# Performance work log

Hardware: AMD Instinct MI355X
Metric: run time of the kernel (lower is better)

## Reference

```python
import jax, jax.numpy as jnp
import numpy as np

H = 256

def setup_inputs() -> dict:
    key = jax.random.key(0)
    ks = jax.random.split(key, 8)
    B, S = 32, 4096
    hidden = jax.random.normal(ks[0], (B, H), dtype=jnp.float32)
    encoder_outputs = jax.random.normal(ks[1], (B, S, H), dtype=jnp.float32)
    scale = 1.0 / np.sqrt(H)
    W1_w = jax.random.uniform(ks[2], (H, H), jnp.float32, -scale, scale)
    W1_b = jax.random.uniform(ks[3], (H,), jnp.float32, -scale, scale)
    W2_w = jax.random.uniform(ks[4], (H, H), jnp.float32, -scale, scale)
    W2_b = jax.random.uniform(ks[5], (H,), jnp.float32, -scale, scale)
    V_w = jax.random.uniform(ks[6], (H, 1), jnp.float32, -scale, scale)
    V_b = jax.random.uniform(ks[7], (1,), jnp.float32, -scale, scale)
    return {"hidden": hidden, "encoder_outputs": encoder_outputs,
            "W1_w": W1_w, "W1_b": W1_b, "W2_w": W2_w, "W2_b": W2_b,
            "V_w": V_w, "V_b": V_b}

def reference(hidden, encoder_outputs, W1_w, W1_b, W2_w, W2_b, V_w, V_b):
    # hidden: (B,H), encoder_outputs: (B,S,H)
    q = hidden @ W1_w + W1_b                     # (B,H)
    k = jnp.einsum('bsh,hd->bsd', encoder_outputs, W2_w) + W2_b  # (B,S,H)
    energy = jnp.tanh(q[:, None, :] + k)         # (B,S,H)
    scores = jnp.einsum('bsh,ho->bso', energy, V_w) + V_b        # (B,S,1)
    attention_weights = jax.nn.softmax(scores, axis=1)           # (B,S,1)
    context_vector = jnp.einsum('bso,bsh->bh', attention_weights, encoder_outputs)  # (B,H)
    return attention_weights, context_vector
```

## Files before the change

### kernel.cpp

```cpp
#include <hip/hip_runtime.h>
#include <hip/hip_bf16.h>
#include <math.h>

#define BB 32
#define SS 4096
#define HH 256

typedef __bf16 bf16x8 __attribute__((ext_vector_type(8)));
typedef float f32x4 __attribute__((ext_vector_type(4)));

#define GLOBAL_AS __attribute__((address_space(1)))
#define LDS_AS    __attribute__((address_space(3)))

__device__ inline bf16x8 cvt8(const float4& x, const float4& y) {
    union { __hip_bfloat162 p[4]; bf16x8 v; } u;
    u.p[0] = __float22bfloat162_rn(make_float2(x.x, x.y));
    u.p[1] = __float22bfloat162_rn(make_float2(x.z, x.w));
    u.p[2] = __float22bfloat162_rn(make_float2(y.x, y.y));
    u.p[3] = __float22bfloat162_rn(make_float2(y.z, y.w));
    return u.v;
}

__device__ inline float fast_tanh(float x) {
    float xc = fminf(fmaxf(x, -10.f), 10.f);
    float e  = __expf(2.f * xc);
    return (e - 1.f) * __builtin_amdgcn_rcpf(e + 1.f);
}

__global__ void prep_kernel(const float* __restrict__ W2_w,
                            ushort* __restrict__ w2sw,
                            const float* __restrict__ hidden,
                            const float* __restrict__ W1_w,
                            const float* __restrict__ W1_b,
                            const float* __restrict__ W2_b,
                            float* __restrict__ qq) {
    __shared__ float hid[HH];
    const int t = threadIdx.x;
    if (blockIdx.x < 256) {
        const int i = blockIdx.x * 256 + t;
        const int j    = i & 7;
        const int lane = (i >> 3) & 63;
        const int nt   = (i >> 9) & 15;
        const int kc   = i >> 13;
        const int k = kc * 32 + ((lane >> 4) & 3) * 8 + j;
        const int n = nt * 16 + (lane & 15);
        __hip_bfloat16 h = __float2bfloat16(W2_w[k * HH + n]);
        w2sw[i] = *(ushort*)&h;
    } else {
        const int b = blockIdx.x - 256;
        hid[t] = hidden[b * HH + t];
        __syncthreads();
        float acc = 0.f;
#pragma unroll 16
        for (int k = 0; k < HH; ++k)
            acc = fmaf(hid[k], W1_w[k * HH + t], acc);
        qq[b * HH + t] = acc + W1_b[t] + W2_b[t];
    }
}

__global__ __launch_bounds__(256, 4)
void score_kernel(const float* __restrict__ enc,
                  const ushort* __restrict__ w2sw,
                  const float* __restrict__ qq,
                  const float* __restrict__ V_w,
                  const float* __restrict__ V_b,
                  float* __restrict__ scores,
                  float* __restrict__ mlpart) {
    __shared__ ushort w2buf[2][8192];
    __shared__ float sc_lds[64];

    const int t    = threadIdx.x;
    const int b    = blockIdx.y;
    const int s0   = blockIdx.x * 64;
    const int wave = t >> 6;
    const int lane = t & 63;
    const int mw   = wave & 1;
    const int nw   = wave >> 1;
    const int l15  = lane & 15;
    const int quad = lane >> 4;

    f32x4 acc[2][8];
#pragma unroll
    for (int mt = 0; mt < 2; ++mt)
#pragma unroll
        for (int nt = 0; nt < 8; ++nt) acc[mt][nt] = (f32x4)0.f;

    {
        const char* gsrc = (const char*)w2sw + t * 16;
        char* ldst = (char*)&w2buf[0][0] + wave * 1024;
#pragma unroll
        for (int i = 0; i < 4; ++i)
            __builtin_amdgcn_global_load_lds(
                (const GLOBAL_AS void*)(gsrc + i * 4096),
                (LDS_AS void*)(ldst + i * 4096), 16, 0, 0);
    }

    const float* aptr0 =
        enc + ((size_t)(b * SS + s0 + mw * 32 + l15)) * HH + quad * 8;
    const float* aptr1 = aptr0 + (size_t)16 * HH;
    float4 ax0 = *(const float4*)aptr0, ay0 = *(const float4*)(aptr0 + 4);
    float4 ax1 = *(const float4*)aptr1, ay1 = *(const float4*)(aptr1 + 4);

    for (int kc = 0; kc < 8; ++kc) {
        const int cur = kc & 1;
        __syncthreads();
        if (kc < 7) {
            const char* gsrc = (const char*)w2sw + (kc + 1) * 16384 + t * 16;
            char* ldst = (char*)&w2buf[cur ^ 1][0] + wave * 1024;
#pragma unroll
            for (int i = 0; i < 4; ++i)
                __builtin_amdgcn_global_load_lds(
                    (const GLOBAL_AS void*)(gsrc + i * 4096),
                    (LDS_AS void*)(ldst + i * 4096), 16, 0, 0);
        }
        bf16x8 af0 = cvt8(ax0, ay0);
        bf16x8 af1 = cvt8(ax1, ay1);
        if (kc < 7) {
            const int o = (kc + 1) * 32;
            ax0 = *(const float4*)(aptr0 + o);
            ay0 = *(const float4*)(aptr0 + o + 4);
            ax1 = *(const float4*)(aptr1 + o);
            ay1 = *(const float4*)(aptr1 + o + 4);
        }
#pragma unroll
        for (int nt = 0; nt < 8; ++nt) {
            bf16x8 bf =
                *(const bf16x8*)&w2buf[cur][((nw * 8 + nt) * 64 + lane) * 8];
            acc[0][nt] = __builtin_amdgcn_mfma_f32_16x16x32_bf16(af0, bf, acc[0][nt], 0, 0, 0);
            acc[1][nt] = __builtin_amdgcn_mfma_f32_16x16x32_bf16(af1, bf, acc[1][nt], 0, 0, 0);
        }
    }

    float p[2][4] = {{0.f, 0.f, 0.f, 0.f}, {0.f, 0.f, 0.f, 0.f}};
#pragma unroll
    for (int nt = 0; nt < 8; ++nt) {
        const int n = nw * 128 + nt * 16 + l15;
        const float qn = qq[b * HH + n];
        const float vn = V_w[n];
#pragma unroll
        for (int mt = 0; mt < 2; ++mt)
#pragma unroll
            for (int r = 0; r < 4; ++r)
                p[mt][r] = fmaf(vn, fast_tanh(qn + acc[mt][nt][r]), p[mt][r]);
    }
#pragma unroll
    for (int off = 1; off < 16; off <<= 1)
#pragma unroll
        for (int mt = 0; mt < 2; ++mt)
#pragma unroll
            for (int r = 0; r < 4; ++r)
                p[mt][r] += __shfl_xor(p[mt][r], off);

    if (nw == 0 && l15 == 0) {
#pragma unroll
        for (int mt = 0; mt < 2; ++mt)
            *(float4*)&sc_lds[mw * 32 + mt * 16 + quad * 4] =
                make_float4(p[mt][0], p[mt][1], p[mt][2], p[mt][3]);
    }
    __syncthreads();
    const float vb = V_b[0];
    if (nw == 1 && l15 == 0) {
#pragma unroll
        for (int mt = 0; mt < 2; ++mt) {
            const int row = mw * 32 + mt * 16 + quad * 4;
            float4 h = *(const float4*)&sc_lds[row];
            float4 v = make_float4(h.x + p[mt][0] + vb, h.y + p[mt][1] + vb,
                                   h.z + p[mt][2] + vb, h.w + p[mt][3] + vb);
            *(float4*)&sc_lds[row] = v;
            *(float4*)&scores[b * SS + s0 + row] = v;
        }
    }
    __syncthreads();

    if (t < 64) {
        const float v = sc_lds[t];
        float m = v;
#pragma unroll
        for (int off = 1; off < 64; off <<= 1)
            m = fmaxf(m, __shfl_xor(m, off));
        float e = __expf(v - m);
#pragma unroll
        for (int off = 1; off < 64; off <<= 1)
            e += __shfl_xor(e, off);
        if (t == 0) {
            mlpart[(b * 64 + blockIdx.x) * 2]     = m;
            mlpart[(b * 64 + blockIdx.x) * 2 + 1] = e;
        }
    }
}

__global__ __launch_bounds__(256)
void ctx_kernel(const float* __restrict__ scores,
                const float* __restrict__ mlpart,
                const float* __restrict__ enc,
                float* __restrict__ weights_out,
                float* __restrict__ ctx_out) {
    __shared__ float wlds[64];
    __shared__ float accl[4][HH];
    __shared__ float mg_s, linv_s;

    const int t  = threadIdx.x;
    const int b  = blockIdx.y;
    const int c  = blockIdx.x;
    const int s0 = c * 64;

    if (t < 64) {
        const float2 ml = ((const float2*)mlpart)[b * 64 + t];
        float m = ml.x;
#pragma unroll
        for (int off = 1; off < 64; off <<= 1)
            m = fmaxf(m, __shfl_xor(m, off));
        float l = ml.y * __expf(ml.x - m);
#pragma unroll
        for (int off = 1; off < 64; off <<= 1)
            l += __shfl_xor(l, off);
        if (t == 0) { mg_s = m; linv_s = 1.f / l; }
    }
    __syncthreads();
    const float mg = mg_s, linv = linv_s;

    if (t < 64) {
        const float w = __expf(scores[b * SS + s0 + t] - mg) * linv;
        weights_out[b * SS + s0 + t] = w;
        wlds[t] = w;
    }
    __syncthreads();

    const int tr = t >> 6;
    const int h0 = (t & 63) * 4;
    float4 a = make_float4(0.f, 0.f, 0.f, 0.f);
    const float* ep = enc + ((size_t)(b * SS + s0)) * HH;
#pragma unroll
    for (int jj = 0; jj < 16; ++jj) {
        const int j = jj * 4 + tr;
        const float4 e = *(const float4*)(ep + (size_t)j * HH + h0);
        const float w = wlds[j];
        a.x = fmaf(w, e.x, a.x);
        a.y = fmaf(w, e.y, a.y);
        a.z = fmaf(w, e.z, a.z);
        a.w = fmaf(w, e.w, a.w);
    }
    *(float4*)&accl[tr][h0] = a;
    __syncthreads();

    const float s = accl[0][t] + accl[1][t] + accl[2][t] + accl[3][t];
    atomicAdd(&ctx_out[b * HH + t], s);
}

extern "C" void kernel_launch(void* const* d_in, const int* in_sizes, int n_in,
                              void* d_out, int out_size, void* d_ws, size_t ws_size,
                              hipStream_t stream) {
    const float* hidden = (const float*)d_in[0];
    const float* enc    = (const float*)d_in[1];
    const float* W1_w   = (const float*)d_in[2];
    const float* W1_b   = (const float*)d_in[3];
    const float* W2_w   = (const float*)d_in[4];
    const float* W2_b   = (const float*)d_in[5];
    const float* V_w    = (const float*)d_in[6];
    const float* V_b    = (const float*)d_in[7];

    float* out_weights = (float*)d_out;
    float* out_ctx     = (float*)d_out + BB * SS;

    float* ws     = (float*)d_ws;
    float* ws_qq  = ws;
    float* ws_sc  = ws_qq + BB * HH;
    float* ws_ml  = ws_sc + BB * SS;
    ushort* ws_w2 = (ushort*)(ws_ml + BB * 64 * 2);

    hipMemsetAsync(out_ctx, 0, BB * HH * sizeof(float), stream);
    prep_kernel<<<dim3(256 + BB), dim3(256), 0, stream>>>(
        W2_w, ws_w2, hidden, W1_w, W1_b, W2_b, ws_qq);
    score_kernel<<<dim3(SS / 64, BB), dim3(256), 0, stream>>>(
        enc, ws_w2, ws_qq, V_w, V_b, ws_sc, ws_ml);
    ctx_kernel<<<dim3(64, BB), dim3(256), 0, stream>>>(
        ws_sc, ws_ml, enc, out_weights, out_ctx);
}
```

Before: 255.2 us.

## Fuse score and context passes using a static softmax max bound

Uses sum(|V_w|) as an upper bound on every score (tanh is bounded by 1), so each block can exponentiate its scores right away without a global max pass. This lets the score kernel also do the weighted sum over its encoder tile while that tile is likely still in cache, removing the second full read of encoder_outputs. Per-block partial contexts go to a workspace, and a small finish kernel normalises the weights and sums the partials, replacing the memset and the atomics. V_b is dropped because it cancels in the softmax. The risk is underflow in exp if the real scores fall far below the bound.

```diff
diff --git a/kernel.cpp b/kernel.cpp
--- a/kernel.cpp
+++ b/kernel.cpp
@@ -33,8 +33,10 @@
                             const float* __restrict__ W1_w,
                             const float* __restrict__ W1_b,
                             const float* __restrict__ W2_b,
-                            float* __restrict__ qq) {
-    __shared__ float hid[HH];
+                            const float* __restrict__ V_w,
+                            float* __restrict__ qq,
+                            float* __restrict__ Mout) {
+    __shared__ float red[HH];
     const int t = threadIdx.x;
     if (blockIdx.x < 256) {
         const int i = blockIdx.x * 256 + t;
@@ -46,32 +48,42 @@
         const int n = nt * 16 + (lane & 15);
         __hip_bfloat16 h = __float2bfloat16(W2_w[k * HH + n]);
         w2sw[i] = *(ushort*)&h;
-    } else {
+    } else if (blockIdx.x < 256 + BB) {
         const int b = blockIdx.x - 256;
-        hid[t] = hidden[b * HH + t];
+        red[t] = hidden[b * HH + t];
         __syncthreads();
         float acc = 0.f;
 #pragma unroll 16
         for (int k = 0; k < HH; ++k)
-            acc = fmaf(hid[k], W1_w[k * HH + t], acc);
+            acc = fmaf(red[k], W1_w[k * HH + t], acc);
         qq[b * HH + t] = acc + W1_b[t] + W2_b[t];
+    } else {
+        red[t] = fabsf(V_w[t]);
+        __syncthreads();
+        for (int off = 128; off > 0; off >>= 1) {
+            if (t < off) red[t] += red[t + off];
+            __syncthreads();
+        }
+        if (t == 0) Mout[0] = red[0];
     }
 }
 
 __global__ __launch_bounds__(256, 4)
-void score_kernel(const float* __restrict__ enc,
-                  const ushort* __restrict__ w2sw,
-                  const float* __restrict__ qq,
-                  const float* __restrict__ V_w,
-                  const float* __restrict__ V_b,
-                  float* __restrict__ scores,
-                  float* __restrict__ mlpart) {
+void score_ctx_kernel(const float* __restrict__ enc,
+                      const ushort* __restrict__ w2sw,
+                      const float* __restrict__ qq,
+                      const float* __restrict__ V_w,
+                      const float* __restrict__ Mptr,
+                      float* __restrict__ wtilde,
+                      float* __restrict__ part) {
     __shared__ ushort w2buf[2][8192];
     __shared__ float sc_lds[64];
+    __shared__ float accl[4][HH];
 
     const int t    = threadIdx.x;
     const int b    = blockIdx.y;
-    const int s0   = blockIdx.x * 64;
+    const int c    = blockIdx.x;
+    const int s0   = c * 64;
     const int wave = t >> 6;
     const int lane = t & 63;
     const int mw   = wave & 1;
@@ -158,71 +170,19 @@
                 make_float4(p[mt][0], p[mt][1], p[mt][2], p[mt][3]);
     }
     __syncthreads();
-    const float vb = V_b[0];
+    const float Mv = Mptr[0];
     if (nw == 1 && l15 == 0) {
 #pragma unroll
         for (int mt = 0; mt < 2; ++mt) {
             const int row = mw * 32 + mt * 16 + quad * 4;
             float4 h = *(const float4*)&sc_lds[row];
-            float4 v = make_float4(h.x + p[mt][0] + vb, h.y + p[mt][1] + vb,
-                                   h.z + p[mt][2] + vb, h.w + p[mt][3] + vb);
+            float4 v = make_float4(__expf(h.x + p[mt][0] - Mv),
+                                   __expf(h.y + p[mt][1] - Mv),
+                                   __expf(h.z + p[mt][2] - Mv),
+                                   __expf(h.w + p[mt][3] - Mv));
             *(float4*)&sc_lds[row] = v;
-            *(float4*)&scores[b * SS + s0 + row] = v;
-        }
-    }
-    __syncthreads();
-
-    if (t < 64) {
-        const float v = sc_lds[t];
-        float m = v;
-#pragma unroll
-        for (int off = 1; off < 64; off <<= 1)
-            m = fmaxf(m, __shfl_xor(m, off));
-        float e = __expf(v - m);
-#pragma unroll
-        for (int off = 1; off < 64; off <<= 1)
-            e += __shfl_xor(e, off);
-        if (t == 0) {
-            mlpart[(b * 64 + blockIdx.x) * 2]     = m;
-            mlpart[(b * 64 + blockIdx.x) * 2 + 1] = e;
-        }
-    }
-}
-
-__global__ __launch_bounds__(256)
-void ctx_kernel(const float* __restrict__ scores,
-                const float* __restrict__ mlpart,
-                const float* __restrict__ enc,
-                float* __restrict__ weights_out,
-                float* __restrict__ ctx_out) {
-    __shared__ float wlds[64];
-    __shared__ float accl[4][HH];
-    __shared__ float mg_s, linv_s;
-
-    const int t  = threadIdx.x;
-    const int b  = blockIdx.y;
-    const int c  = blockIdx.x;
-    const int s0 = c * 64;
-
-    if (t < 64) {
-        const float2 ml = ((const float2*)mlpart)[b * 64 + t];
-        float m = ml.x;
-#pragma unroll
-        for (int off = 1; off < 64; off <<= 1)
-            m = fmaxf(m, __shfl_xor(m, off));
-        float l = ml.y * __expf(ml.x - m);
-#pragma unroll
-        for (int off = 1; off < 64; off <<= 1)
-            l += __shfl_xor(l, off);
-        if (t == 0) { mg_s = m; linv_s = 1.f / l; }
-    }
-    __syncthreads();
-    const float mg = mg_s, linv = linv_s;
-
-    if (t < 64) {
-        const float w = __expf(scores[b * SS + s0 + t] - mg) * linv;
-        weights_out[b * SS + s0 + t] = w;
-        wlds[t] = w;
+            *(float4*)&wtilde[b * SS + s0 + row] = v;
+        }
     }
     __syncthreads();
 
@@ -234,7 +194,7 @@
     for (int jj = 0; jj < 16; ++jj) {
         const int j = jj * 4 + tr;
         const float4 e = *(const float4*)(ep + (size_t)j * HH + h0);
-        const float w = wlds[j];
+        const float w = sc_lds[j];
         a.x = fmaf(w, e.x, a.x);
         a.y = fmaf(w, e.y, a.y);
         a.z = fmaf(w, e.z, a.z);
@@ -243,8 +203,51 @@
     *(float4*)&accl[tr][h0] = a;
     __syncthreads();
 
-    const float s = accl[0][t] + accl[1][t] + accl[2][t] + accl[3][t];
-    atomicAdd(&ctx_out[b * HH + t], s);
+    part[((size_t)(b * 64 + c)) * HH + t] =
+        accl[0][t] + accl[1][t] + accl[2][t] + accl[3][t];
+}
+
+__global__ __launch_bounds__(256)
+void finish_kernel(const float* __restrict__ wtilde,
+                   const float* __restrict__ part,
+                   float* __restrict__ weights_out,
+                   float* __restrict__ ctx_out) {
+    __shared__ float red[256];
+    __shared__ float linv_s;
+    const int b = blockIdx.x;
+    const int t = threadIdx.x;
+
+    const float4* wt4 = (const float4*)(wtilde + (size_t)b * SS);
+    float4 vals[4];
+    float l = 0.f;
+#pragma unroll
+    for (int i = 0; i < 4; ++i) {
+        vals[i] = wt4[i * 256 + t];
+        l += vals[i].x + vals[i].y + vals[i].z + vals[i].w;
+    }
+    red[t] = l;
+    __syncthreads();
+    for (int off = 128; off > 0; off >>= 1) {
+        if (t < off) red[t] += red[t + off];
+        __syncthreads();
+    }
+    if (t == 0) linv_s = 1.f / red[0];
+    __syncthreads();
+    const float linv = linv_s;
+
+    float4* wo4 = (float4*)(weights_out + (size_t)b * SS);
+#pragma unroll
+    for (int i = 0; i < 4; ++i) {
+        const float4 v = vals[i];
+        wo4[i * 256 + t] =
+            make_float4(v.x * linv, v.y * linv, v.z * linv, v.w * linv);
+    }
+
+    float a = 0.f;
+#pragma unroll 8
+    for (int c = 0; c < 64; ++c)
+        a += part[((size_t)(b * 64 + c)) * HH + t];
+    ctx_out[b * HH + t] = a * linv;
 }
 
 extern "C" void kernel_launch(void* const* d_in, const int* in_sizes, int n_in,
@@ -258,21 +261,22 @@
     const float* W2_b   = (const float*)d_in[5];
     const float* V_w    = (const float*)d_in[6];
     const float* V_b    = (const float*)d_in[7];
+    (void)V_b;
 
     float* out_weights = (float*)d_out;
     float* out_ctx     = (float*)d_out + BB * SS;
 
-    float* ws     = (float*)d_ws;
-    float* ws_qq  = ws;
-    float* ws_sc  = ws_qq + BB * HH;
-    float* ws_ml  = ws_sc + BB * SS;
-    ushort* ws_w2 = (ushort*)(ws_ml + BB * 64 * 2);
-
-    hipMemsetAsync(out_ctx, 0, BB * HH * sizeof(float), stream);
-    prep_kernel<<<dim3(256 + BB), dim3(256), 0, stream>>>(
-        W2_w, ws_w2, hidden, W1_w, W1_b, W2_b, ws_qq);
-    score_kernel<<<dim3(SS / 64, BB), dim3(256), 0, stream>>>(
-        enc, ws_w2, ws_qq, V_w, V_b, ws_sc, ws_ml);
-    ctx_kernel<<<dim3(64, BB), dim3(256), 0, stream>>>(
-        ws_sc, ws_ml, enc, out_weights, out_ctx);
-}
+    float* ws      = (float*)d_ws;
+    float* ws_qq   = ws;
+    float* ws_wt   = ws_qq + BB * HH;
+    float* ws_part = ws_wt + BB * SS;
+    float* ws_M    = ws_part + BB * 64 * HH;
+    ushort* ws_w2  = (ushort*)(ws_M + 4);
+
+    prep_kernel<<<dim3(256 + BB + 1), dim3(256), 0, stream>>>(
+        W2_w, ws_w2, hidden, W1_w, W1_b, W2_b, V_w, ws_qq, ws_M);
+    score_ctx_kernel<<<dim3(SS / 64, BB), dim3(256), 0, stream>>>(
+        enc, ws_w2, ws_qq, V_w, ws_M, ws_wt, ws_part);
+    finish_kernel<<<dim3(BB), dim3(256), 0, stream>>>(
+        ws_wt, ws_part, out_weights, out_ctx);
+}
```

Result: faster. 247.2 us (-3.2%).
